# Performance work log

Measured on AMD Instinct MI355X. Metric: run time of the kernel, lower is better.

## Reference

```python
import jax, jax.numpy as jnp
import numpy as np

B, H, S, D = 512, 1024, 1024, 128
TOPK = 32

def setup_inputs() -> dict:
    key = jax.random.key(0)
    ks = jax.random.split(key, 12)
    w = lambda k, shape: (jax.random.normal(k, shape, dtype=jnp.float32) * 0.02)
    return {
        "latent": jax.random.normal(ks[0], (B, H), dtype=jnp.float32),
        "memory": jax.random.normal(ks[1], (B, S, D), dtype=jnp.float32),
        "read_query_w": w(ks[2], (H, D)),
        "read_query_b": jnp.zeros((D,), jnp.float32),
        "memory_key": w(ks[3], (S, D)),
        "write_gate_w": w(ks[4], (H + D, 1)),
        "write_gate_b": jnp.zeros((1,), jnp.float32),
        "dmd_proj_w": w(ks[5], (H + D, 1)),
        "dmd_proj_b": jnp.zeros((1,), jnp.float32),
        "phase_proj_w": w(ks[6], (H, 1)),
        "phase_proj_b": jnp.zeros((1,), jnp.float32),
        "write_value_w": w(ks[7], (H, D)),
        "write_value_b": jnp.zeros((D,), jnp.float32),
    }

def reference(latent, memory, read_query_w, read_query_b, memory_key,
              write_gate_w, write_gate_b, dmd_proj_w, dmd_proj_b,
              phase_proj_w, phase_proj_b, write_value_w, write_value_b):
    # soft read over memory slots
    query = latent @ read_query_w + read_query_b              # [B, D]
    logits = jnp.einsum('bd,sd->bs', query, memory_key)       # [B, S]
    weights = jax.nn.softmax(logits, axis=-1)
    # top-k masked renormalization (topk=32 < S)
    _, topk_idx = jax.lax.top_k(weights, TOPK)                # [B, K]
    rows = jnp.arange(weights.shape[0])[:, None]
    mask = jnp.zeros_like(weights).at[rows, topk_idx].set(1.0)
    weights = weights * mask
    weights = weights / jnp.clip(weights.sum(-1, keepdims=True), 1e-8)
    read = jnp.einsum('bs,bsd->bd', weights, memory)          # [B, D]
    gate_input = jnp.concatenate([latent, read], axis=-1)     # [B, H+D]
    # sigmoid gate (gating_mode='sigmoid')
    gate = jax.nn.sigmoid(gate_input @ write_gate_w + write_gate_b)  # [B, 1]
    # dmd gating
    dmd_signal = jnp.tanh(gate_input @ dmd_proj_w + dmd_proj_b)
    gate = jnp.clip(gate * (0.75 + 0.5 * (dmd_signal + 1.0) * 0.5), 0.0, 1.0)
    # phase gating
    phase = latent @ phase_proj_w + phase_proj_b
    gate = gate * (0.5 * (1.0 + jnp.cos(phase)))
    # soft scatter-write update
    value = (latent @ write_value_w + write_value_b)[:, None, :]      # [B, 1, D]
    gw = gate[:, :, None] * weights[:, :, None]                       # [B, S, 1]
    new_memory = (1.0 - gw) * memory + gw * value                     # [B, S, D]
    return read, new_memory, weights
```

## Files before the change

### kernel.cpp

```cpp
#include <hip/hip_runtime.h>
#include <math.h>

#define NB 512
#define NH 1024
#define NS 1024
#define ND 128
#define NK 32

typedef float fx4 __attribute__((ext_vector_type(4)));

__device__ __forceinline__ void bar_lgkm() {
  asm volatile("s_waitcnt lgkmcnt(0)" ::: "memory");
  __builtin_amdgcn_s_barrier();
  __builtin_amdgcn_sched_barrier(0);
}
__device__ __forceinline__ void bar_full() {
  asm volatile("s_waitcnt vmcnt(0) lgkmcnt(0)" ::: "memory");
  __builtin_amdgcn_s_barrier();
  __builtin_amdgcn_sched_barrier(0);
}

__global__ __launch_bounds__(512, 4) void fused_kernel(
    const float* __restrict__ latent,
    const float* __restrict__ memory,
    const float* __restrict__ rq_w,
    const float* __restrict__ rq_b,
    const float* __restrict__ mem_key,
    const float* __restrict__ wg_w,
    const float* __restrict__ wg_b,
    const float* __restrict__ dmd_w,
    const float* __restrict__ dmd_b,
    const float* __restrict__ ph_w,
    const float* __restrict__ ph_b,
    const float* __restrict__ wv_w,
    const float* __restrict__ wv_b,
    float* __restrict__ out_read,
    float* __restrict__ out_mem,
    float* __restrict__ out_wts)
{
  const int b    = blockIdx.x;
  const int tid  = threadIdx.x;
  const int lane = tid & 63;
  const int wv   = tid >> 6;

  __shared__ float lat[NH];
  __shared__ float wfull[NS];
  __shared__ float part[512];
  __shared__ __align__(16) float qv[ND];
  __shared__ float rd[ND];
  __shared__ float tvw[256];
  __shared__ int   tiw[256];
  __shared__ float wkL[NK];
  __shared__ int   tiL[NK];
  __shared__ __align__(16) float valw_s[ND];
  __shared__ float gred[24];
  __shared__ float scal[1];

  const fx4* __restrict__ msrc = (const fx4*)memory + (size_t)b * (NS * ND / 4);
  fx4*       __restrict__ mdst = (fx4*)out_mem      + (size_t)b * (NS * ND / 4);
  fx4 bufA[8], bufB[8];
  int cur_l = 0, cur_s = 0;

#define CK_LOAD(BUF, N)  { _Pragma("unroll") \
    for (int j = 0; j < (N); ++j) \
      BUF[j] = __builtin_nontemporal_load(msrc + (size_t)(cur_l + j) * 512 + tid); \
    cur_l += (N); }
#define CK_STORE(BUF, N) { _Pragma("unroll") \
    for (int j = 0; j < (N); ++j) \
      __builtin_nontemporal_store(BUF[j], mdst + (size_t)(cur_s + j) * 512 + tid); \
    cur_s += (N); }

  CK_LOAD(bufA, 8);
  lat[tid]       = latent[(size_t)b * NH + tid];
  lat[tid + 512] = latent[(size_t)b * NH + tid + 512];
  bar_lgkm();

  CK_LOAD(bufB, 4);
  CK_STORE(bufA, 8);
  {
    const int d = tid & 127, p = tid >> 7;
    const float* W = rq_w + (size_t)(p * 256) * ND + d;
    const float* L = lat + p * 256;
    float acc = 0.f;
    #pragma unroll 8
    for (int h = 0; h < 256; ++h) acc = fmaf(L[h], W[(size_t)h * ND], acc);
    part[tid] = acc;
  }
  bar_lgkm();

  CK_LOAD(bufA, 8);
  CK_STORE(bufB, 4);
  if (tid < ND)
    qv[tid] = part[tid] + part[tid + 128] + part[tid + 256] + part[tid + 384] + rq_b[tid];
  bar_lgkm();

  CK_LOAD(bufB, 8);
  CK_STORE(bufA, 8);
  float r0 = 0.f, r1 = 0.f;
  {
    const float4* q4 = (const float4*)qv;
    const float4* k0 = (const float4*)(mem_key + (size_t)tid * ND);
    const float4* k1 = (const float4*)(mem_key + (size_t)(tid + 512) * ND);
    #pragma unroll 8
    for (int i = 0; i < ND / 4; ++i) {
      float4 q = q4[i];
      float4 x = k0[i];
      float4 y = k1[i];
      r0 += q.x * x.x + q.y * x.y + q.z * x.z + q.w * x.w;
      r1 += q.x * y.x + q.y * y.y + q.z * y.z + q.w * y.w;
    }
  }
  const float NEGINF = -3.0e38f;
  float selv = NEGINF; int seli = -1; float wkreg = 0.f;
  {
    const int s0 = tid, s1 = tid + 512;
    float v0 = r0, v1 = r1;
    for (int kk = 0; kk < NK; ++kk) {
      float best; int bi;
      if (v0 >= v1) { best = v0; bi = s0; } else { best = v1; bi = s1; }
      #pragma unroll
      for (int off = 1; off < 64; off <<= 1) {
        float ov = __shfl_xor(best, off);
        int   oi = __shfl_xor(bi, off);
        if (ov > best || (ov == best && oi < bi)) { best = ov; bi = oi; }
      }
      if (lane == 0) { tvw[(wv << 5) + kk] = best; tiw[(wv << 5) + kk] = bi; }
      if (bi == s0) v0 = NEGINF;
      if (bi == s1) v1 = NEGINF;
    }
  }
  wfull[tid] = 0.f; wfull[tid + 512] = 0.f;
  bar_lgkm();

  CK_LOAD(bufA, 8);
  CK_STORE(bufB, 8);
  if (wv == 0) {
    float m0 = tvw[lane], m1 = tvw[lane + 64], m2 = tvw[lane + 128], m3 = tvw[lane + 192];
    int   i0 = tiw[lane], i1 = tiw[lane + 64], i2 = tiw[lane + 128], i3 = tiw[lane + 192];
    for (int kk = 0; kk < NK; ++kk) {
      float best = m0; int bi = i0;
      if (m1 > best || (m1 == best && i1 < bi)) { best = m1; bi = i1; }
      if (m2 > best || (m2 == best && i2 < bi)) { best = m2; bi = i2; }
      if (m3 > best || (m3 == best && i3 < bi)) { best = m3; bi = i3; }
      #pragma unroll
      for (int off = 1; off < 64; off <<= 1) {
        float ov = __shfl_xor(best, off);
        int   oi = __shfl_xor(bi, off);
        if (ov > best || (ov == best && oi < bi)) { best = ov; bi = oi; }
      }
      if (kk == lane) { selv = best; seli = bi; }
      if (bi == i0) m0 = NEGINF;
      if (bi == i1) m1 = NEGINF;
      if (bi == i2) m2 = NEGINF;
      if (bi == i3) m3 = NEGINF;
    }
    float maxv = __shfl(selv, 0);
    float e = (lane < NK) ? expf(selv - maxv) : 0.f;
    float s = e;
    #pragma unroll
    for (int off = 1; off < 64; off <<= 1) s += __shfl_xor(s, off);
    wkreg = e / s;
    if (lane < NK) { wkL[lane] = wkreg; tiL[lane] = seli; }
  }
  bar_lgkm();

  CK_LOAD(bufB, 4);
  CK_STORE(bufA, 8);
  if (wv == 0 && lane < NK) wfull[seli] = wkreg;
  {
    const int d = tid & 127, p = tid >> 7;
    const float* mb = memory + (size_t)b * NS * ND;
    float racc = 0.f;
    #pragma unroll
    for (int k = p * 8; k < p * 8 + 8; ++k)
      racc = fmaf(wkL[k], mb[(size_t)tiL[k] * ND + d], racc);
    part[tid] = racc;
  }
  bar_lgkm();

  CK_LOAD(bufA, 8);
  CK_STORE(bufB, 4);
  if (tid < ND) {
    float r = part[tid] + part[tid + 128] + part[tid + 256] + part[tid + 384];
    rd[tid] = r;
    out_read[(size_t)b * ND + tid] = r;
  }
  bar_lgkm();

  CK_LOAD(bufB, 4);
  CK_STORE(bufA, 8);
  {
    float l0 = lat[tid], l1 = lat[tid + 512];
    float p1 = l0 * wg_w[tid]  + l1 * wg_w[tid + 512];
    float p2 = l0 * dmd_w[tid] + l1 * dmd_w[tid + 512];
    float p3 = l0 * ph_w[tid]  + l1 * ph_w[tid + 512];
    if (tid < ND) {
      float r = rd[tid];
      p1 += r * wg_w[NH + tid];
      p2 += r * dmd_w[NH + tid];
    }
    #pragma unroll
    for (int off = 1; off < 64; off <<= 1) {
      p1 += __shfl_xor(p1, off);
      p2 += __shfl_xor(p2, off);
      p3 += __shfl_xor(p3, off);
    }
    if (lane == 0) { gred[wv] = p1; gred[8 + wv] = p2; gred[16 + wv] = p3; }
  }
  {
    const int d = tid & 127, p = tid >> 7;
    const float* W = wv_w + (size_t)(p * 256) * ND + d;
    const float* L = lat + p * 256;
    float acc = 0.f;
    #pragma unroll 8
    for (int h = 0; h < 256; ++h) acc = fmaf(L[h], W[(size_t)h * ND], acc);
    part[tid] = acc;
  }
  bar_lgkm();

  CK_LOAD(bufA, 6);
  CK_STORE(bufB, 4);
  if (tid == 0) {
    float z1 = wg_b[0], z2 = dmd_b[0], z3 = ph_b[0];
    #pragma unroll
    for (int k = 0; k < 8; ++k) { z1 += gred[k]; z2 += gred[8 + k]; z3 += gred[16 + k]; }
    float g  = 1.f / (1.f + expf(-z1));
    float dm = tanhf(z2);
    g = g * (0.75f + 0.25f * (dm + 1.f));
    g = fminf(fmaxf(g, 0.f), 1.f);
    g = g * (0.5f * (1.f + cosf(z3)));
    scal[0] = g;
  }
  bar_lgkm();

  CK_LOAD(bufB, 6);
  CK_STORE(bufA, 6);
  {
    float w0 = wfull[tid], w1 = wfull[tid + 512];
    out_wts[(size_t)b * NS + tid]       = w0;
    out_wts[(size_t)b * NS + tid + 512] = w1;
    if (tid < ND)
      valw_s[tid] = part[tid] + part[tid + 128] + part[tid + 256] + part[tid + 384] + wv_b[tid];
  }
  bar_lgkm();

  CK_STORE(bufB, 6);
  bar_full();
  {
    const float g = scal[0];
    const fx4* v4 = (const fx4*)valw_s;
    #pragma unroll
    for (int u = 0; u < 2; ++u) {
      const int idx = tid + u * 512;
      const int k   = idx >> 5;
      const int c   = idx & 31;
      const float w = g * wkL[k];
      const int row = tiL[k];
      const fx4 m = msrc[(size_t)row * 32 + c];
      __builtin_nontemporal_store((1.f - w) * m + w * v4[c],
                                  mdst + (size_t)row * 32 + c);
    }
  }
#undef CK_LOAD
#undef CK_STORE
}

extern "C" void kernel_launch(void* const* d_in, const int* in_sizes, int n_in,
                              void* d_out, int out_size, void* d_ws, size_t ws_size,
                              hipStream_t stream) {
  const float* latent  = (const float*)d_in[0];
  const float* memory  = (const float*)d_in[1];
  const float* rq_w    = (const float*)d_in[2];
  const float* rq_b    = (const float*)d_in[3];
  const float* mem_key = (const float*)d_in[4];
  const float* wg_w    = (const float*)d_in[5];
  const float* wg_b    = (const float*)d_in[6];
  const float* dmd_w   = (const float*)d_in[7];
  const float* dmd_b   = (const float*)d_in[8];
  const float* ph_w    = (const float*)d_in[9];
  const float* ph_b    = (const float*)d_in[10];
  const float* wv_w    = (const float*)d_in[11];
  const float* wv_b    = (const float*)d_in[12];

  float* out_read = (float*)d_out;
  float* out_mem  = out_read + (size_t)NB * ND;
  float* out_wts  = out_mem + (size_t)NB * NS * ND;

  fused_kernel<<<NB, 512, 0, stream>>>(
      latent, memory, rq_w, rq_b, mem_key, wg_w, wg_b, dmd_w, dmd_b,
      ph_w, ph_b, wv_w, wv_b, out_read, out_mem, out_wts);
}
```

Before: 523.2 us.

## Vectorize small GEMVs and side loads with float4, drop sched barriers

Rewrites the latent-by-weight GEMVs (read query, write value) so each thread accumulates a float4 of output columns over a 64-row slice, and reduces across 16 partial slices. The top-k read gather, the latent load, the gate dot products and the weights output now use 128-bit accesses. It also removes the sched_barrier after each barrier, which lets the compiler move instructions across the streaming copy phases. This cuts the instruction count and memory transaction count of the compute side-work that is interleaved with the memory copy, at the cost of more LDS reduction steps and possibly less control over how the copy loads and stores are scheduled.

```diff
diff --git a/kernel.cpp b/kernel.cpp
--- a/kernel.cpp
+++ b/kernel.cpp
@@ -12,12 +12,10 @@
 __device__ __forceinline__ void bar_lgkm() {
   asm volatile("s_waitcnt lgkmcnt(0)" ::: "memory");
   __builtin_amdgcn_s_barrier();
-  __builtin_amdgcn_sched_barrier(0);
 }
 __device__ __forceinline__ void bar_full() {
   asm volatile("s_waitcnt vmcnt(0) lgkmcnt(0)" ::: "memory");
   __builtin_amdgcn_s_barrier();
-  __builtin_amdgcn_sched_barrier(0);
 }
 
 __global__ __launch_bounds__(512, 4) void fused_kernel(
@@ -43,9 +41,9 @@
   const int lane = tid & 63;
   const int wv   = tid >> 6;
 
-  __shared__ float lat[NH];
-  __shared__ float wfull[NS];
-  __shared__ float part[512];
+  __shared__ __align__(16) float lat[NH];
+  __shared__ __align__(16) float wfull[NS];
+  __shared__ __align__(16) fx4   part4[512];
   __shared__ __align__(16) float qv[ND];
   __shared__ float rd[ND];
   __shared__ float tvw[256];
@@ -56,6 +54,8 @@
   __shared__ float gred[24];
   __shared__ float scal[1];
 
+  float* part4f = (float*)part4;
+
   const fx4* __restrict__ msrc = (const fx4*)memory + (size_t)b * (NS * ND / 4);
   fx4*       __restrict__ mdst = (fx4*)out_mem      + (size_t)b * (NS * ND / 4);
   fx4 bufA[8], bufB[8];
@@ -70,28 +70,41 @@
       __builtin_nontemporal_store(BUF[j], mdst + (size_t)(cur_s + j) * 512 + tid); \
     cur_s += (N); }
 
+  const int og = tid & 31;
+  const int pp = tid >> 5;
+  const fx4* lat4 = (const fx4*)lat;
+
   CK_LOAD(bufA, 8);
-  lat[tid]       = latent[(size_t)b * NH + tid];
-  lat[tid + 512] = latent[(size_t)b * NH + tid + 512];
+  if (tid < 256)
+    ((fx4*)lat)[tid] = ((const fx4*)(latent + (size_t)b * NH))[tid];
   bar_lgkm();
 
   CK_LOAD(bufB, 4);
   CK_STORE(bufA, 8);
   {
-    const int d = tid & 127, p = tid >> 7;
-    const float* W = rq_w + (size_t)(p * 256) * ND + d;
-    const float* L = lat + p * 256;
-    float acc = 0.f;
-    #pragma unroll 8
-    for (int h = 0; h < 256; ++h) acc = fmaf(L[h], W[(size_t)h * ND], acc);
-    part[tid] = acc;
+    const fx4* W4 = (const fx4*)rq_w;
+    fx4 acc = {0.f, 0.f, 0.f, 0.f};
+    const int hbase = pp * 64;
+    #pragma unroll 4
+    for (int j = 0; j < 16; ++j) {
+      fx4 l4 = lat4[(hbase >> 2) + j];
+      acc += l4.x * W4[(size_t)(hbase + 4*j    ) * 32 + og];
+      acc += l4.y * W4[(size_t)(hbase + 4*j + 1) * 32 + og];
+      acc += l4.z * W4[(size_t)(hbase + 4*j + 2) * 32 + og];
+      acc += l4.w * W4[(size_t)(hbase + 4*j + 3) * 32 + og];
+    }
+    part4[pp * 32 + og] = acc;
   }
   bar_lgkm();
 
   CK_LOAD(bufA, 8);
   CK_STORE(bufB, 4);
-  if (tid < ND)
-    qv[tid] = part[tid] + part[tid + 128] + part[tid + 256] + part[tid + 384] + rq_b[tid];
+  if (tid < ND) {
+    float q = rq_b[tid];
+    #pragma unroll
+    for (int p = 0; p < 16; ++p) q += part4f[p * 128 + tid];
+    qv[tid] = q;
+  }
   bar_lgkm();
 
   CK_LOAD(bufB, 8);
@@ -168,20 +181,20 @@
   CK_STORE(bufA, 8);
   if (wv == 0 && lane < NK) wfull[seli] = wkreg;
   {
-    const int d = tid & 127, p = tid >> 7;
-    const float* mb = memory + (size_t)b * NS * ND;
-    float racc = 0.f;
-    #pragma unroll
-    for (int k = p * 8; k < p * 8 + 8; ++k)
-      racc = fmaf(wkL[k], mb[(size_t)tiL[k] * ND + d], racc);
-    part[tid] = racc;
+    const fx4* mb4 = (const fx4*)(memory + (size_t)b * NS * ND);
+    const int k0i = pp, k1i = pp + 16;
+    fx4 racc = wkL[k0i] * mb4[(size_t)tiL[k0i] * 32 + og]
+             + wkL[k1i] * mb4[(size_t)tiL[k1i] * 32 + og];
+    part4[pp * 32 + og] = racc;
   }
   bar_lgkm();
 
   CK_LOAD(bufA, 8);
   CK_STORE(bufB, 4);
   if (tid < ND) {
-    float r = part[tid] + part[tid + 128] + part[tid + 256] + part[tid + 384];
+    float r = 0.f;
+    #pragma unroll
+    for (int p = 0; p < 16; ++p) r += part4f[p * 128 + tid];
     rd[tid] = r;
     out_read[(size_t)b * ND + tid] = r;
   }
@@ -190,14 +203,20 @@
   CK_LOAD(bufB, 4);
   CK_STORE(bufA, 8);
   {
-    float l0 = lat[tid], l1 = lat[tid + 512];
-    float p1 = l0 * wg_w[tid]  + l1 * wg_w[tid + 512];
-    float p2 = l0 * dmd_w[tid] + l1 * dmd_w[tid + 512];
-    float p3 = l0 * ph_w[tid]  + l1 * ph_w[tid + 512];
-    if (tid < ND) {
-      float r = rd[tid];
-      p1 += r * wg_w[NH + tid];
-      p2 += r * dmd_w[NH + tid];
+    float p1 = 0.f, p2 = 0.f, p3 = 0.f;
+    if (tid < 256) {
+      fx4 l4 = lat4[tid];
+      fx4 a = ((const fx4*)wg_w)[tid];
+      fx4 d4 = ((const fx4*)dmd_w)[tid];
+      fx4 c4 = ((const fx4*)ph_w)[tid];
+      p1 = l4.x*a.x + l4.y*a.y + l4.z*a.z + l4.w*a.w;
+      p2 = l4.x*d4.x + l4.y*d4.y + l4.z*d4.z + l4.w*d4.w;
+      p3 = l4.x*c4.x + l4.y*c4.y + l4.z*c4.z + l4.w*c4.w;
+    } else if (tid < 384) {
+      const int d = tid - 256;
+      float r = rd[d];
+      p1 = r * wg_w[NH + d];
+      p2 = r * dmd_w[NH + d];
     }
     #pragma unroll
     for (int off = 1; off < 64; off <<= 1) {
@@ -208,13 +227,18 @@
     if (lane == 0) { gred[wv] = p1; gred[8 + wv] = p2; gred[16 + wv] = p3; }
   }
   {
-    const int d = tid & 127, p = tid >> 7;
-    const float* W = wv_w + (size_t)(p * 256) * ND + d;
-    const float* L = lat + p * 256;
-    float acc = 0.f;
-    #pragma unroll 8
-    for (int h = 0; h < 256; ++h) acc = fmaf(L[h], W[(size_t)h * ND], acc);
-    part[tid] = acc;
+    const fx4* W4 = (const fx4*)wv_w;
+    fx4 acc = {0.f, 0.f, 0.f, 0.f};
+    const int hbase = pp * 64;
+    #pragma unroll 4
+    for (int j = 0; j < 16; ++j) {
+      fx4 l4 = lat4[(hbase >> 2) + j];
+      acc += l4.x * W4[(size_t)(hbase + 4*j    ) * 32 + og];
+      acc += l4.y * W4[(size_t)(hbase + 4*j + 1) * 32 + og];
+      acc += l4.z * W4[(size_t)(hbase + 4*j + 2) * 32 + og];
+      acc += l4.w * W4[(size_t)(hbase + 4*j + 3) * 32 + og];
+    }
+    part4[pp * 32 + og] = acc;
   }
   bar_lgkm();
 
@@ -235,12 +259,13 @@
 
   CK_LOAD(bufB, 6);
   CK_STORE(bufA, 6);
-  {
-    float w0 = wfull[tid], w1 = wfull[tid + 512];
-    out_wts[(size_t)b * NS + tid]       = w0;
-    out_wts[(size_t)b * NS + tid + 512] = w1;
-    if (tid < ND)
-      valw_s[tid] = part[tid] + part[tid + 128] + part[tid + 256] + part[tid + 384] + wv_b[tid];
+  if (tid < 256)
+    ((fx4*)(out_wts + (size_t)b * NS))[tid] = ((const fx4*)wfull)[tid];
+  if (tid < ND) {
+    float v = wv_b[tid];
+    #pragma unroll
+    for (int p = 0; p < 16; ++p) v += part4f[p * 128 + tid];
+    valw_s[tid] = v;
   }
   bar_lgkm();
 
```

After: 507.1 us. -3.1%, faster.
